# Kernel tuning notes

Measured on AMD Instinct MI355X. Metric: run time of the kernel, lower is better.

Reference implementation:

```python
import jax, jax.numpy as jnp
import numpy as np

EPS = 1e-5
NUM_GROUPS = 32


def group_norm(x, num_groups=NUM_GROUPS, eps=EPS):
    # x: [B, C, H, W]; normalize over (C//G, H, W) per group, no affine
    B, C, H, W = x.shape
    xg = x.reshape(B, num_groups, C // num_groups, H, W)
    mean = xg.mean(axis=(2, 3, 4), keepdims=True)
    var = xg.var(axis=(2, 3, 4), keepdims=True)
    xg = (xg - mean) * jax.lax.rsqrt(var + eps)
    return xg.reshape(B, C, H, W)


def nin(x, W, b):
    # 1x1 dense projection over channel dim: [B,C,H,W] x [C,O] -> [B,O,H,W]
    return jnp.einsum('bchw,co->bohw', x, W) + b[None, :, None, None]


def setup_inputs() -> dict:
    key = jax.random.key(0)
    ks = jax.random.split(key, 9)
    B, C, H, W_ = 32, 512, 32, 32
    s = 1.0 / np.sqrt(C)
    return {
        'x': jax.random.normal(ks[0], (B, C, H, W_), jnp.float32),
        'Wq': jax.random.normal(ks[1], (C, C), jnp.float32) * s,
        'bq': jnp.zeros((C,), jnp.float32),
        'Wk': jax.random.normal(ks[2], (C, C), jnp.float32) * s,
        'bk': jnp.zeros((C,), jnp.float32),
        'Wv': jax.random.normal(ks[3], (C, C), jnp.float32) * s,
        'bv': jnp.zeros((C,), jnp.float32),
        'Wn': jax.random.normal(ks[4], (C, C), jnp.float32) * (0.05 * s),
        'bn': jnp.zeros((C,), jnp.float32),
    }


def reference(x, Wq, bq, Wk, bk, Wv, bv, Wn, bn):
    B, C, H, W_ = x.shape
    h = group_norm(x)
    q = nin(h, Wq, bq)
    k = nin(h, Wk, bk)
    v = nin(h, Wv, bv)
    scale = jnp.asarray(C, x.dtype) ** -0.5
    # full spatial attention: [B, H, W, H', W']
    w = jnp.einsum('bchw,bcHW->bhwHW', q, k) * scale
    w = w.reshape(B, H, W_, H * W_)
    w = jax.nn.softmax(w, axis=-1)
    w = w.reshape(B, H, W_, H, W_)
    h = jnp.einsum('bhwHW,bcHW->bchw', w, v)
    h = nin(h, Wn, bn)
    return x + h
```

## Files before the change

kernel.cpp:

```cpp
#include <hip/hip_runtime.h>
#include <cstdint>

#define B_   32
#define C_   512
#define N_   1024
#define G_   32
#define CG_  16

typedef unsigned short u16;
typedef unsigned char u8;
typedef unsigned long long u64;

static constexpr float kEps = 1e-5f;
static constexpr float kLog2Scale = 0.06375871752987579f;

using f32x4  = __attribute__((ext_vector_type(4))) float;
using short8 = __attribute__((ext_vector_type(8))) short;
using i64x2  = __attribute__((ext_vector_type(2))) long long;

__device__ __forceinline__ u16 f2bf(float f) {
  uint32_t u = __builtin_bit_cast(uint32_t, f);
  u += 0x7fffu + ((u >> 16) & 1u);
  return (u16)(u >> 16);
}
__device__ __forceinline__ int pk4_fp8(float a, float b, float c, float d) {
  int w = __builtin_amdgcn_cvt_pk_fp8_f32(a, b, 0, false);
  w = __builtin_amdgcn_cvt_pk_fp8_f32(c, d, w, true);
  return w;
}
__device__ __forceinline__ int f8pos(int k) {
  const int c8 = (k >> 3) & 7;
  return (k & ~63) + ((c8 & 3) << 4) + ((c8 >> 2) << 3) + (k & 4);
}

__device__ __forceinline__ void gload16(const void* g, void* lds) {
  __builtin_amdgcn_global_load_lds(
      (__attribute__((address_space(1))) void*)(uintptr_t)g,
      (__attribute__((address_space(3))) void*)(uint32_t)(uintptr_t)lds,
      16, 0, 0);
}

__device__ __forceinline__ uint3 remap_xcd() {
  const int gx = gridDim.x, gy = gridDim.y, gz = gridDim.z;
  const int nwg = gx * gy * gz;
  const int lin = blockIdx.x + gx * (blockIdx.y + gy * blockIdx.z);
  const int q = nwg >> 3, r = nwg & 7;
  const int xcd = lin & 7, pos = lin >> 3;
  int nid = (xcd < r ? xcd * (q + 1) : r * (q + 1) + (xcd - r) * q) + pos;
  uint3 o;
  o.x = nid % gx; nid /= gx;
  o.y = nid % gy; o.z = nid / gy;
  return o;
}

__global__ __launch_bounds__(256) void wcvt_kernel(
    const float* __restrict__ Wq, const float* __restrict__ Wk,
    const float* __restrict__ Wv, u16* __restrict__ Wab, u16* __restrict__ Wbb) {
  const int idx = blockIdx.x * 256 + threadIdx.x;
  const int src = idx >> 16;
  const int e = (idx & 65535) * 4;
  const float* W = (src == 0) ? Wq : (src == 1) ? Wk : Wv;
  u16* D = (src == 0) ? Wab : (src == 1) ? Wbb : (Wab + 262144);
  const float4 v = *(const float4*)(W + e);
  ushort4 st;
  st.x = f2bf(v.x); st.y = f2bf(v.y); st.z = f2bf(v.z); st.w = f2bf(v.w);
  *(ushort4*)(D + e) = st;
}

__global__ __launch_bounds__(256) void wtr_kernel(
    const float* __restrict__ Wn, u16* __restrict__ Wtn) {
  __shared__ float tile[64][65];
  const int c0 = blockIdx.y * 64, o0 = blockIdx.x * 64;
  const int tx = threadIdx.x & 15, ty = threadIdx.x >> 4;
#pragma unroll
  for (int rr = 0; rr < 64; rr += 16) {
    const int c = c0 + ty + rr;
    const float4 v = *(const float4*)(Wn + (size_t)c * 512 + o0 + tx * 4);
    tile[ty + rr][tx * 4 + 0] = v.x;
    tile[ty + rr][tx * 4 + 1] = v.y;
    tile[ty + rr][tx * 4 + 2] = v.z;
    tile[ty + rr][tx * 4 + 3] = v.w;
  }
  __syncthreads();
#pragma unroll
  for (int rr = 0; rr < 64; rr += 16) {
    const int o = o0 + ty + rr;
    ushort4 st;
    st.x = f2bf(tile[tx * 4 + 0][ty + rr]);
    st.y = f2bf(tile[tx * 4 + 1][ty + rr]);
    st.z = f2bf(tile[tx * 4 + 2][ty + rr]);
    st.w = f2bf(tile[tx * 4 + 3][ty + rr]);
    *(ushort4*)(Wtn + (size_t)o * 512 + c0 + tx * 4) = st;
  }
}

__global__ __launch_bounds__(512) void biask_kernel(
    const float* __restrict__ Wk, const float* __restrict__ bq,
    const float* __restrict__ Wn, const float* __restrict__ bv,
    const float* __restrict__ bn, float* __restrict__ wkbq,
    float* __restrict__ bvn) {
  const int t = threadIdx.x;
  if (blockIdx.x == 0) {
    float s = 0.f;
    const float* row = Wk + (size_t)t * 512;
    for (int o = 0; o < 512; ++o) s += row[o] * bq[o];
    wkbq[t] = s;
  } else {
    float s = 0.f;
    for (int c = 0; c < 512; ++c) s += bv[c] * Wn[(size_t)c * 512 + t];
    bvn[t] = s + bn[t];
  }
}

__global__ __launch_bounds__(256) void gn_fused(const float* __restrict__ x,
                                                u8* __restrict__ Hn8,
                                                u8* __restrict__ HnT8) {
  __shared__ float lds[16 * 1028];
  __shared__ float red[10];
  const int bg = blockIdx.x, b = bg >> 5, g = bg & 31;
  const int t = threadIdx.x;
  const float4* p4 = (const float4*)(x + (size_t)bg * 16384);
  float s = 0.f, s2 = 0.f;
  for (int i = t; i < 4096; i += 256) {
    const float4 v = p4[i];
    const int e = i * 4, ic = e >> 10, n = e & 1023;
    *(float4*)(lds + ic * 1028 + n) = v;
    s  += v.x + v.y + v.z + v.w;
    s2 += v.x * v.x + v.y * v.y + v.z * v.z + v.w * v.w;
  }
#pragma unroll
  for (int o = 32; o; o >>= 1) { s += __shfl_xor(s, o); s2 += __shfl_xor(s2, o); }
  const int lane = t & 63, w = t >> 6;
  if (lane == 0) { red[w] = s; red[4 + w] = s2; }
  __syncthreads();
  if (t == 0) {
    s  = red[0] + red[1] + red[2] + red[3];
    s2 = red[4] + red[5] + red[6] + red[7];
    const float inv = 1.0f / 16384.0f;
    const float mean = s * inv;
    const float var  = s2 * inv - mean * mean;
    red[8] = mean;
    red[9] = rsqrtf(var + kEps);
  }
  __syncthreads();
  const float mean = red[8], rstd = red[9];
#pragma unroll
  for (int r = 0; r < 4; ++r) {
    const int n = t + 256 * r;
    float vals[16];
#pragma unroll
    for (int ic = 0; ic < 16; ++ic)
      vals[ic] = (lds[ic * 1028 + n] - mean) * rstd;
    const u64 lo = (u64)(uint32_t)pk4_fp8(vals[0], vals[1], vals[2], vals[3]) |
                   ((u64)(uint32_t)pk4_fp8(vals[4], vals[5], vals[6], vals[7]) << 32);
    const u64 hi = (u64)(uint32_t)pk4_fp8(vals[8], vals[9], vals[10], vals[11]) |
                   ((u64)(uint32_t)pk4_fp8(vals[12], vals[13], vals[14], vals[15]) << 32);
    u8* rb = Hn8 + ((size_t)(b * N_ + n)) * C_;
    *(u64*)(rb + f8pos(g * 16))     = lo;
    *(u64*)(rb + f8pos(g * 16 + 8)) = hi;
  }
  const int nb = t * 4;
#pragma unroll
  for (int ic = 0; ic < 16; ++ic) {
    const int wv = pk4_fp8((lds[ic * 1028 + nb + 0] - mean) * rstd,
                           (lds[ic * 1028 + nb + 1] - mean) * rstd,
                           (lds[ic * 1028 + nb + 2] - mean) * rstd,
                           (lds[ic * 1028 + nb + 3] - mean) * rstd);
    *(int*)(HnT8 + ((size_t)(b * C_ + g * 16 + ic)) * N_ + f8pos(nb)) = wv;
  }
}

__global__ __launch_bounds__(256) void gemm_w128(
    const u16* __restrict__ Ab, const u16* __restrict__ Bb, u8* __restrict__ Ob) {
  __shared__ u16 Alds[128 * 64];
  __shared__ u16 Blds[128 * 64];
  const int p = blockIdx.z;
  const u16* A = Ab + (size_t)p * 262144;
  const u16* B = Bb + (size_t)p * 262144;
  u8* O = Ob + (size_t)p * 262144;
  const int m0 = blockIdx.y * 128, n0 = blockIdx.x * 128;
  const int tid = threadIdx.x, lane = tid & 63, wid = tid >> 6;
  const int wm = wid >> 1, wn = wid & 1;
  const int sr = lane >> 3, scb = (lane & 7) ^ sr;
  const u16* Ag = A + (size_t)(m0 + wid * 32 + sr) * 512 + scb * 8;
  const u16* Bg = B + (size_t)(n0 + wid * 32 + sr) * 512 + scb * 8;
  char* Al = (char*)Alds + wid * 4096;
  char* Bl = (char*)Blds + wid * 4096;
  const int arow = lane & 15, g4 = lane >> 4, rx = lane & 7;
  f32x4 acc[4][4] = {};
  for (int k = 0; k < 512; k += 64) {
#pragma unroll
    for (int g = 0; g < 4; ++g) {
      gload16(Ag + k + g * (8 * 512), Al + g * 1024);
      gload16(Bg + k + g * (8 * 512), Bl + g * 1024);
    }
    __syncthreads();
#pragma unroll
    for (int kk = 0; kk < 2; ++kk) {
      const int pc = ((kk * 4 + g4) ^ rx) * 16;
      short8 a[4], b[4];
#pragma unroll
      for (int i = 0; i < 4; ++i)
        a[i] = *(const short8*)((const char*)Alds + (wm * 64 + i * 16 + arow) * 128 + pc);
#pragma unroll
      for (int j = 0; j < 4; ++j)
        b[j] = *(const short8*)((const char*)Blds + (wn * 64 + j * 16 + arow) * 128 + pc);
#pragma unroll
      for (int i = 0; i < 4; ++i)
#pragma unroll
        for (int j = 0; j < 4; ++j)
          acc[i][j] = __builtin_amdgcn_mfma_f32_16x16x32_bf16(a[i], b[j], acc[i][j], 0, 0, 0);
    }
    __syncthreads();
  }
#pragma unroll
  for (int i = 0; i < 4; ++i) {
    const int rowg = m0 + wm * 64 + i * 16 + ((lane >> 4) * 4);
#pragma unroll
    for (int j = 0; j < 4; ++j) {
      const int colg = n0 + wn * 64 + j * 16 + (lane & 15);
      const f32x4 v = acc[i][j];
      *(int*)(O + (size_t)colg * 512 + f8pos(rowg)) =
          pk4_fp8(v[0], v[1], v[2], v[3]);
    }
  }
}

#define LDA8_(D, BASE, MH)                                                      \
  _Pragma("unroll")                                                             \
  for (int i_ = 0; i_ < 4; ++i_) {                                              \
    const int rr_ = wm * 128 + (MH) * 64 + i_ * 16 + arow;                      \
    D[i_] = *(const i64x2*)((BASE) + rr_ * 64 +                                 \
                            ((g4 ^ ((rr_ >> 1) & 3)) << 4));                    \
  }
#define LDB8_(D, BASE)                                                          \
  _Pragma("unroll")                                                             \
  for (int j_ = 0; j_ < 4; ++j_) {                                              \
    const int rr_ = wn * 64 + j_ * 16 + arow;                                   \
    D[j_] = *(const i64x2*)((BASE) + rr_ * 64 +                                 \
                            ((g4 ^ ((rr_ >> 1) & 3)) << 4));                    \
  }
#define MM8_(ACC, AA, BB, H)                                                    \
  __builtin_amdgcn_s_setprio(1);                                                \
  _Pragma("unroll")                                                             \
  for (int i_ = 0; i_ < 4; ++i_)                                                \
    _Pragma("unroll")                                                           \
    for (int j_ = 0; j_ < 4; ++j_)                                              \
      ACC[i_][j_] = __builtin_amdgcn_mfma_f32_16x16x32_fp8_fp8(                 \
          AA[i_][H], BB[j_][H], ACC[i_][j_], 0, 0, 0);                          \
  __builtin_amdgcn_s_setprio(0);

__device__ __forceinline__ void gemm_core256_f8(
    const u8* __restrict__ A, const u8* __restrict__ B,
    int Ktot, int m0, int n0,
    char* Alds, char* Blds, f32x4 acc0[4][4], f32x4 acc1[4][4]) {
  const int tid = threadIdx.x, lane = tid & 63, wid = tid >> 6;
  const int wm = wid >> 2, wn = wid & 3;
  const int rl = lane >> 2;
  const int c16 = (lane & 3) ^ ((lane >> 3) & 3);
  const u8* Ag = A + (size_t)(m0 + wid * 32 + rl) * Ktot + c16 * 16;
  const u8* Bg = B + (size_t)(n0 + wid * 32 + rl) * Ktot + c16 * 16;
  char* Al = Alds + wid * 2048;
  char* Bl = Blds + wid * 2048;
  const long long r16 = (long long)16 * Ktot;
  const int arow = lane & 15, g4 = lane >> 4;
  const int nt = Ktot >> 6;

#pragma unroll
  for (int g = 0; g < 2; ++g) {
    gload16(Ag + g * r16, Al + g * 1024);
    gload16(Bg + g * r16, Bl + g * 1024);
  }
  asm volatile("s_waitcnt vmcnt(0)" ::: "memory");
  __builtin_amdgcn_s_barrier();
  i64x2 aX[4], aY[4], bX[4];
  LDA8_(aX, Alds, 0);

  for (int t = 0; t < nt; ++t) {
    const int cur = t & 1;
    const char* Ab = Alds + cur * 16384;
    const char* Bb = Blds + cur * 16384;
    const char* An = Alds + (cur ^ 1) * 16384;
    char* Aln = Al + (cur ^ 1) * 16384;
    char* Bln = Bl + (cur ^ 1) * 16384;
    const bool nx = (t + 1 < nt);
    const long long ko = (long long)(t + 1) * 64;

    if (nx) {
#pragma unroll
      for (int g = 0; g < 2; ++g) gload16(Bg + ko + g * r16, Bln + g * 1024);
    }
    LDB8_(bX, Bb);
    LDA8_(aY, Ab, 1);
    asm volatile("s_waitcnt lgkmcnt(4)" ::: "memory");
    __builtin_amdgcn_sched_barrier(0);
    __builtin_amdgcn_s_barrier();
    MM8_(acc0, aX, bX, 0);

    if (nx) {
#pragma unroll
      for (int g = 0; g < 2; ++g) gload16(Ag + ko + g * r16, Aln + g * 1024);
    }
    asm volatile("s_waitcnt lgkmcnt(0)" ::: "memory");
    __builtin_amdgcn_sched_barrier(0);
    __builtin_amdgcn_s_barrier();
    MM8_(acc1, aY, bX, 0);

    __builtin_amdgcn_sched_barrier(0);
    __builtin_amdgcn_s_barrier();
    MM8_(acc0, aX, bX, 1);

    if (nx) {
      asm volatile("s_waitcnt vmcnt(0)" ::: "memory");
    }
    __builtin_amdgcn_sched_barrier(0);
    __builtin_amdgcn_s_barrier();
    if (nx) {
      LDA8_(aX, An, 0);
    }
    MM8_(acc1, aY, bX, 1);
  }
}

__global__ __launch_bounds__(512, 2) void gemm_hwq_f8(
    const u8* __restrict__ Wqk8, const u8* __restrict__ Hn8,
    const float* __restrict__ wkbq, u8* __restrict__ HWq8) {
  __shared__ char Alds[2 * 256 * 64];
  __shared__ char Blds[2 * 256 * 64];
  const uint3 bid = remap_xcd();
  const int z = bid.z;
  const u8* B = Hn8 + (size_t)z * ((size_t)N_ * C_);
  u8* O = HWq8 + (size_t)z * ((size_t)N_ * C_);
  const int m0 = bid.y * 256, n0 = bid.x * 256;
  f32x4 acc0[4][4] = {};
  f32x4 acc1[4][4] = {};
  gemm_core256_f8(Wqk8, B, 512, m0, n0, Alds, Blds, acc0, acc1);

  const int lane = threadIdx.x & 63, wid = threadIdx.x >> 6;
  const int wm = wid >> 2, wn = wid & 3;
#pragma unroll
  for (int i = 0; i < 8; ++i) {
    const int rowg = m0 + wm * 128 + i * 16 + ((lane >> 4) * 4);
    const float4 bv = *(const float4*)(wkbq + rowg);
#pragma unroll
    for (int j = 0; j < 4; ++j) {
      const int colg = n0 + wn * 64 + j * 16 + (lane & 15);
      const f32x4 v = (i < 4) ? acc0[i][j] : acc1[i - 4][j];
      *(int*)(O + (size_t)colg * 512 + f8pos(rowg)) =
          pk4_fp8(v[0] + bv.x, v[1] + bv.y, v[2] + bv.z, v[3] + bv.w);
    }
  }
}

__global__ __launch_bounds__(512, 2) void gemm_s_f8(
    const u8* __restrict__ Hn8, const u8* __restrict__ HWq8,
    u8* __restrict__ P8, float* __restrict__ Psum) {
  __shared__ char Alds[2 * 256 * 64];
  __shared__ char Blds[2 * 256 * 64];
  const uint3 bid = remap_xcd();
  const int z = bid.z;
  const u8* A = Hn8  + (size_t)z * ((size_t)N_ * C_);
  const u8* B = HWq8 + (size_t)z * ((size_t)N_ * C_);
  u8*       O = P8   + (size_t)z * ((size_t)N_ * N_);
  const int m0 = bid.y * 256, n0 = bid.x * 256;
  f32x4 acc0[4][4] = {};
  f32x4 acc1[4][4] = {};
  gemm_core256_f8(A, B, 512, m0, n0, Alds, Blds, acc0, acc1);

  const int lane = threadIdx.x & 63, wid = threadIdx.x >> 6;
  const int wm = wid >> 2, wn = wid & 3;
  float psum[4] = {0.f, 0.f, 0.f, 0.f};
#pragma unroll
  for (int i = 0; i < 8; ++i) {
    const int rowg = m0 + wm * 128 + i * 16 + ((lane >> 4) * 4);
#pragma unroll
    for (int j = 0; j < 4; ++j) {
      const int colg = n0 + wn * 64 + j * 16 + (lane & 15);
      const f32x4 v = (i < 4) ? acc0[i][j] : acc1[i - 4][j];
      const float p0 = __builtin_exp2f(v[0] * kLog2Scale) * 0.0625f;
      const float p1 = __builtin_exp2f(v[1] * kLog2Scale) * 0.0625f;
      const float p2 = __builtin_exp2f(v[2] * kLog2Scale) * 0.0625f;
      const float p3 = __builtin_exp2f(v[3] * kLog2Scale) * 0.0625f;
      psum[j] += (p0 + p1) + (p2 + p3);
      *(int*)(O + (size_t)colg * 1024 + f8pos(rowg)) = pk4_fp8(p0, p1, p2, p3);
    }
  }
  const int slot = (m0 >> 7) + wm;
  float* Ps = Psum + ((size_t)z * 8 + slot) * N_;
#pragma unroll
  for (int j = 0; j < 4; ++j) {
    float r = psum[j];
    r += __shfl_xor(r, 16);
    r += __shfl_xor(r, 32);
    if (lane < 16) Ps[n0 + wn * 64 + j * 16 + lane] = r;
  }
}

__global__ __launch_bounds__(512, 2) void gemm_pv_f8(
    const u8* __restrict__ HnT8, const u8* __restrict__ P8,
    const float* __restrict__ Psum, u8* __restrict__ H28) {
  __shared__ char Alds[2 * 256 * 64];
  __shared__ char Blds[2 * 256 * 64];
  const uint3 bid = remap_xcd();
  const int z = bid.z;
  const u8* A = HnT8 + (size_t)z * ((size_t)N_ * C_);
  const u8* B = P8   + (size_t)z * ((size_t)N_ * N_);
  u8*       O = H28  + (size_t)z * ((size_t)N_ * C_);
  const int m0 = bid.y * 256, n0 = bid.x * 256;
  f32x4 acc0[4][4] = {};
  f32x4 acc1[4][4] = {};
  gemm_core256_f8(A, B, 1024, m0, n0, Alds, Blds, acc0, acc1);

  const int lane = threadIdx.x & 63, wid = threadIdx.x >> 6;
  const int wm = wid >> 2, wn = wid & 3;
  const float* Ps = Psum + (size_t)z * 8 * N_;
  float inv[4];
#pragma unroll
  for (int j = 0; j < 4; ++j) {
    const int colg = n0 + wn * 64 + j * 16 + (lane & 15);
    float s = 0.f;
#pragma unroll
    for (int k = 0; k < 8; ++k) s += Ps[k * N_ + colg];
    inv[j] = 1.0f / s;
  }
#pragma unroll
  for (int i = 0; i < 8; ++i) {
    const int rowg = m0 + wm * 128 + i * 16 + ((lane >> 4) * 4);
#pragma unroll
    for (int j = 0; j < 4; ++j) {
      const int colg = n0 + wn * 64 + j * 16 + (lane & 15);
      const f32x4 v = (i < 4) ? acc0[i][j] : acc1[i - 4][j];
      *(int*)(O + (size_t)colg * 512 + f8pos(rowg)) =
          pk4_fp8(v[0] * inv[j], v[1] * inv[j], v[2] * inv[j], v[3] * inv[j]);
    }
  }
}

__global__ __launch_bounds__(512, 2) void gemm_final_f8(
    const u8* __restrict__ H28, const u8* __restrict__ Wvn8,
    const float* __restrict__ x, const float* __restrict__ bvn,
    float* __restrict__ Out) {
  __shared__ char Alds[2 * 256 * 64];
  __shared__ char Blds[2 * 256 * 64];
  const uint3 bid = remap_xcd();
  const int z = bid.z;
  const u8*    Ab = H28 + (size_t)z * ((size_t)N_ * C_);
  const float* xb = x + (size_t)z * ((size_t)C_ * N_);
  float*       Ob = Out + (size_t)z * ((size_t)C_ * N_);
  const int m0 = bid.y * 256, n0 = bid.x * 256;
  f32x4 acc0[4][4] = {};
  f32x4 acc1[4][4] = {};
  gemm_core256_f8(Ab, Wvn8, 512, m0, n0, Alds, Blds, acc0, acc1);

  const int lane = threadIdx.x & 63, wid = threadIdx.x >> 6;
  const int wm = wid >> 2, wn = wid & 3;
#pragma unroll
  for (int i = 0; i < 8; ++i) {
    const int rowg = m0 + wm * 128 + i * 16 + ((lane >> 4) * 4);
#pragma unroll
    for (int j = 0; j < 4; ++j) {
      const int colg = n0 + wn * 64 + j * 16 + (lane & 15);
      const float bc = bvn[colg];
      const size_t off = (size_t)colg * N_ + rowg;
      const float4 xv = *(const float4*)(xb + off);
      const f32x4 v = (i < 4) ? acc0[i][j] : acc1[i - 4][j];
      float4 ov;
      ov.x = xv.x + v[0] + bc;
      ov.y = xv.y + v[1] + bc;
      ov.z = xv.z + v[2] + bc;
      ov.w = xv.w + v[3] + bc;
      *(float4*)(Ob + off) = ov;
    }
  }
}

__global__ void sentinel_kernel(float* out, int n, float v) {
  const int i = blockIdx.x * blockDim.x + threadIdx.x;
  if (i < n) out[i] = v;
}

extern "C" void kernel_launch(void* const* d_in, const int* in_sizes, int n_in,
                              void* d_out, int out_size, void* d_ws, size_t ws_size,
                              hipStream_t stream) {
  const float* x  = (const float*)d_in[0];
  const float* Wq = (const float*)d_in[1];
  const float* bq = (const float*)d_in[2];
  const float* Wk = (const float*)d_in[3];
  const float* Wv = (const float*)d_in[5];
  const float* bv = (const float*)d_in[6];
  const float* Wn = (const float*)d_in[7];
  const float* bn = (const float*)d_in[8];
  float* out = (float*)d_out;

  char* ws = (char*)d_ws;
  size_t off = 0;
  u16* Wab = (u16*)(ws + off); off += (size_t)2 * 262144 * 2;
  u16* Wbb = (u16*)(ws + off); off += (size_t)2 * 262144 * 2;
  u8*  W8  = (u8*)(ws + off);  off += (size_t)2 * 262144;
  float* wkbq = (float*)(ws + off); off += 512 * 4;
  float* bvn  = (float*)(ws + off); off += 512 * 4;
  const size_t bnc = (size_t)B_ * N_ * C_;
  u8* Hn8  = (u8*)(ws + off); off += bnc;
  u8* HnT8 = (u8*)(ws + off); off += bnc;
  u8* HWq8 = (u8*)(ws + off); off += bnc;
  u8* P8   = (u8*)(ws + off); off += (size_t)B_ * N_ * N_;
  u8* H28  = (u8*)(ws + off); off += bnc;
  float* Psum = (float*)(ws + off); off += (size_t)B_ * 8 * N_ * 4;

  if (ws_size < off) {
    const float v = 1.0e6f + (float)(ws_size >> 20);
    sentinel_kernel<<<(out_size + 255) / 256, 256, 0, stream>>>(out, out_size, v);
    return;
  }

  wcvt_kernel<<<768, 256, 0, stream>>>(Wq, Wk, Wv, Wab, Wbb);
  wtr_kernel<<<dim3(8, 8), 256, 0, stream>>>(Wn, Wbb + 262144);
  biask_kernel<<<2, 512, 0, stream>>>(Wk, bq, Wn, bv, bn, wkbq, bvn);
  gn_fused<<<B_ * G_, 256, 0, stream>>>(x, Hn8, HnT8);
  gemm_w128<<<dim3(4, 4, 2), 256, 0, stream>>>(Wab, Wbb, W8);
  gemm_hwq_f8<<<dim3(4, 2, B_), 512, 0, stream>>>(W8, Hn8, wkbq, HWq8);
  gemm_s_f8<<<dim3(4, 4, B_), 512, 0, stream>>>(Hn8, HWq8, P8, Psum);
  gemm_pv_f8<<<dim3(4, 2, B_), 512, 0, stream>>>(HnT8, P8, Psum, H28);
  gemm_final_f8<<<dim3(2, 4, B_), 512, 0, stream>>>(H28, W8 + 262144, x, bvn, out);
}
```

Measured before the change: 203.7 us.

## Stage fp8 GEMM epilogues through LDS for coalesced stores; bf16 LDS in groupnorm

Three fp8 GEMM kernels (hwq, s, pv) now write their packed fp8 output tile into shared memory, which reuses the A/B staging buffers, and then copy it to global memory as 16-byte row-contiguous stores. Previously each lane scattered 4-byte stores with a large stride. The groupnorm kernel also stores the staged input in LDS as bf16 instead of fp32, halving its LDS footprint so more blocks can fit per CU. In exchange this adds two block barriers per GEMM epilogue and rounds the normalized values through bf16 before the fp8 conversion, which slightly changes numerics.

```diff
diff --git a/kernel.cpp b/kernel.cpp
--- a/kernel.cpp
+++ b/kernel.cpp
@@ -22,6 +22,9 @@
   uint32_t u = __builtin_bit_cast(uint32_t, f);
   u += 0x7fffu + ((u >> 16) & 1u);
   return (u16)(u >> 16);
+}
+__device__ __forceinline__ float bf2f(u16 h) {
+  return __builtin_bit_cast(float, (uint32_t)h << 16);
 }
 __device__ __forceinline__ int pk4_fp8(float a, float b, float c, float d) {
   int w = __builtin_amdgcn_cvt_pk_fp8_f32(a, b, 0, false);
@@ -115,7 +118,7 @@
 __global__ __launch_bounds__(256) void gn_fused(const float* __restrict__ x,
                                                 u8* __restrict__ Hn8,
                                                 u8* __restrict__ HnT8) {
-  __shared__ float lds[16 * 1028];
+  __shared__ u16 lds2[16 * 1032];
   __shared__ float red[10];
   const int bg = blockIdx.x, b = bg >> 5, g = bg & 31;
   const int t = threadIdx.x;
@@ -124,7 +127,9 @@
   for (int i = t; i < 4096; i += 256) {
     const float4 v = p4[i];
     const int e = i * 4, ic = e >> 10, n = e & 1023;
-    *(float4*)(lds + ic * 1028 + n) = v;
+    ushort4 sv;
+    sv.x = f2bf(v.x); sv.y = f2bf(v.y); sv.z = f2bf(v.z); sv.w = f2bf(v.w);
+    *(ushort4*)(lds2 + ic * 1032 + n) = sv;
     s  += v.x + v.y + v.z + v.w;
     s2 += v.x * v.x + v.y * v.y + v.z * v.z + v.w * v.w;
   }
@@ -150,7 +155,7 @@
     float vals[16];
 #pragma unroll
     for (int ic = 0; ic < 16; ++ic)
-      vals[ic] = (lds[ic * 1028 + n] - mean) * rstd;
+      vals[ic] = (bf2f(lds2[ic * 1032 + n]) - mean) * rstd;
     const u64 lo = (u64)(uint32_t)pk4_fp8(vals[0], vals[1], vals[2], vals[3]) |
                    ((u64)(uint32_t)pk4_fp8(vals[4], vals[5], vals[6], vals[7]) << 32);
     const u64 hi = (u64)(uint32_t)pk4_fp8(vals[8], vals[9], vals[10], vals[11]) |
@@ -162,10 +167,9 @@
   const int nb = t * 4;
 #pragma unroll
   for (int ic = 0; ic < 16; ++ic) {
-    const int wv = pk4_fp8((lds[ic * 1028 + nb + 0] - mean) * rstd,
-                           (lds[ic * 1028 + nb + 1] - mean) * rstd,
-                           (lds[ic * 1028 + nb + 2] - mean) * rstd,
-                           (lds[ic * 1028 + nb + 3] - mean) * rstd);
+    const ushort4 hv = *(const ushort4*)(lds2 + ic * 1032 + nb);
+    const int wv = pk4_fp8((bf2f(hv.x) - mean) * rstd, (bf2f(hv.y) - mean) * rstd,
+                           (bf2f(hv.z) - mean) * rstd, (bf2f(hv.w) - mean) * rstd);
     *(int*)(HnT8 + ((size_t)(b * C_ + g * 16 + ic)) * N_ + f8pos(nb)) = wv;
   }
 }
@@ -322,11 +326,22 @@
   }
 }
 
+__device__ __forceinline__ void copy_out_tile(const char* SH, u8* O, int LDC,
+                                              int m0, int n0) {
+  const int tid = threadIdx.x;
+#pragma unroll
+  for (int it = 0; it < 8; ++it) {
+    const int flat = it * 8192 + tid * 16;
+    const int row = flat >> 8, col = flat & 255;
+    *(int4*)(O + (size_t)(n0 + row) * LDC + m0 + col) =
+        *(const int4*)(SH + row * 256 + col);
+  }
+}
+
 __global__ __launch_bounds__(512, 2) void gemm_hwq_f8(
     const u8* __restrict__ Wqk8, const u8* __restrict__ Hn8,
     const float* __restrict__ wkbq, u8* __restrict__ HWq8) {
-  __shared__ char Alds[2 * 256 * 64];
-  __shared__ char Blds[2 * 256 * 64];
+  __shared__ char SH[4 * 256 * 64];
   const uint3 bid = remap_xcd();
   const int z = bid.z;
   const u8* B = Hn8 + (size_t)z * ((size_t)N_ * C_);
@@ -334,29 +349,31 @@
   const int m0 = bid.y * 256, n0 = bid.x * 256;
   f32x4 acc0[4][4] = {};
   f32x4 acc1[4][4] = {};
-  gemm_core256_f8(Wqk8, B, 512, m0, n0, Alds, Blds, acc0, acc1);
+  gemm_core256_f8(Wqk8, B, 512, m0, n0, SH, SH + 32768, acc0, acc1);
 
   const int lane = threadIdx.x & 63, wid = threadIdx.x >> 6;
   const int wm = wid >> 2, wn = wid & 3;
+  __syncthreads();
 #pragma unroll
   for (int i = 0; i < 8; ++i) {
-    const int rowg = m0 + wm * 128 + i * 16 + ((lane >> 4) * 4);
-    const float4 bv = *(const float4*)(wkbq + rowg);
+    const int ml = wm * 128 + i * 16 + ((lane >> 4) * 4);
+    const float4 bv = *(const float4*)(wkbq + m0 + ml);
 #pragma unroll
     for (int j = 0; j < 4; ++j) {
-      const int colg = n0 + wn * 64 + j * 16 + (lane & 15);
+      const int nl = wn * 64 + j * 16 + (lane & 15);
       const f32x4 v = (i < 4) ? acc0[i][j] : acc1[i - 4][j];
-      *(int*)(O + (size_t)colg * 512 + f8pos(rowg)) =
+      *(int*)(SH + nl * 256 + f8pos(ml)) =
           pk4_fp8(v[0] + bv.x, v[1] + bv.y, v[2] + bv.z, v[3] + bv.w);
     }
   }
+  __syncthreads();
+  copy_out_tile(SH, O, 512, m0, n0);
 }
 
 __global__ __launch_bounds__(512, 2) void gemm_s_f8(
     const u8* __restrict__ Hn8, const u8* __restrict__ HWq8,
     u8* __restrict__ P8, float* __restrict__ Psum) {
-  __shared__ char Alds[2 * 256 * 64];
-  __shared__ char Blds[2 * 256 * 64];
+  __shared__ char SH[4 * 256 * 64];
   const uint3 bid = remap_xcd();
   const int z = bid.z;
   const u8* A = Hn8  + (size_t)z * ((size_t)N_ * C_);
@@ -365,24 +382,25 @@
   const int m0 = bid.y * 256, n0 = bid.x * 256;
   f32x4 acc0[4][4] = {};
   f32x4 acc1[4][4] = {};
-  gemm_core256_f8(A, B, 512, m0, n0, Alds, Blds, acc0, acc1);
+  gemm_core256_f8(A, B, 512, m0, n0, SH, SH + 32768, acc0, acc1);
 
   const int lane = threadIdx.x & 63, wid = threadIdx.x >> 6;
   const int wm = wid >> 2, wn = wid & 3;
   float psum[4] = {0.f, 0.f, 0.f, 0.f};
+  __syncthreads();
 #pragma unroll
   for (int i = 0; i < 8; ++i) {
-    const int rowg = m0 + wm * 128 + i * 16 + ((lane >> 4) * 4);
+    const int ml = wm * 128 + i * 16 + ((lane >> 4) * 4);
 #pragma unroll
     for (int j = 0; j < 4; ++j) {
-      const int colg = n0 + wn * 64 + j * 16 + (lane & 15);
+      const int nl = wn * 64 + j * 16 + (lane & 15);
       const f32x4 v = (i < 4) ? acc0[i][j] : acc1[i - 4][j];
       const float p0 = __builtin_exp2f(v[0] * kLog2Scale) * 0.0625f;
       const float p1 = __builtin_exp2f(v[1] * kLog2Scale) * 0.0625f;
       const float p2 = __builtin_exp2f(v[2] * kLog2Scale) * 0.0625f;
       const float p3 = __builtin_exp2f(v[3] * kLog2Scale) * 0.0625f;
       psum[j] += (p0 + p1) + (p2 + p3);
-      *(int*)(O + (size_t)colg * 1024 + f8pos(rowg)) = pk4_fp8(p0, p1, p2, p3);
+      *(int*)(SH + nl * 256 + f8pos(ml)) = pk4_fp8(p0, p1, p2, p3);
     }
   }
   const int slot = (m0 >> 7) + wm;
@@ -394,13 +412,14 @@
     r += __shfl_xor(r, 32);
     if (lane < 16) Ps[n0 + wn * 64 + j * 16 + lane] = r;
   }
+  __syncthreads();
+  copy_out_tile(SH, O, 1024, m0, n0);
 }
 
 __global__ __launch_bounds__(512, 2) void gemm_pv_f8(
     const u8* __restrict__ HnT8, const u8* __restrict__ P8,
     const float* __restrict__ Psum, u8* __restrict__ H28) {
-  __shared__ char Alds[2 * 256 * 64];
-  __shared__ char Blds[2 * 256 * 64];
+  __shared__ char SH[4 * 256 * 64];
   const uint3 bid = remap_xcd();
   const int z = bid.z;
   const u8* A = HnT8 + (size_t)z * ((size_t)N_ * C_);
@@ -409,7 +428,7 @@
   const int m0 = bid.y * 256, n0 = bid.x * 256;
   f32x4 acc0[4][4] = {};
   f32x4 acc1[4][4] = {};
-  gemm_core256_f8(A, B, 1024, m0, n0, Alds, Blds, acc0, acc1);
+  gemm_core256_f8(A, B, 1024, m0, n0, SH, SH + 32768, acc0, acc1);
 
   const int lane = threadIdx.x & 63, wid = threadIdx.x >> 6;
   const int wm = wid >> 2, wn = wid & 3;
@@ -423,17 +442,20 @@
     for (int k = 0; k < 8; ++k) s += Ps[k * N_ + colg];
     inv[j] = 1.0f / s;
   }
+  __syncthreads();
 #pragma unroll
   for (int i = 0; i < 8; ++i) {
-    const int rowg = m0 + wm * 128 + i * 16 + ((lane >> 4) * 4);
+    const int ml = wm * 128 + i * 16 + ((lane >> 4) * 4);
 #pragma unroll
     for (int j = 0; j < 4; ++j) {
-      const int colg = n0 + wn * 64 + j * 16 + (lane & 15);
+      const int nl = wn * 64 + j * 16 + (lane & 15);
       const f32x4 v = (i < 4) ? acc0[i][j] : acc1[i - 4][j];
-      *(int*)(O + (size_t)colg * 512 + f8pos(rowg)) =
+      *(int*)(SH + nl * 256 + f8pos(ml)) =
           pk4_fp8(v[0] * inv[j], v[1] * inv[j], v[2] * inv[j], v[3] * inv[j]);
     }
   }
+  __syncthreads();
+  copy_out_tile(SH, O, 512, m0, n0);
 }
 
 __global__ __launch_bounds__(512, 2) void gemm_final_f8(
```

Measured after the change: 194.7 us. 4.4% less time.
